# Kernel tuning notes

Hardware: AMD Instinct MI355X
Metric: run time of the kernel (lower is better)

## Reference

```python
import jax, jax.numpy as jnp
import numpy as np

# Static config (matches init_kwargs)
B, T, D = 4, 2048, 1024
E = 8            # num_experts
K = 2            # top_k
S = 1            # num_shared_experts
H = 1408         # expert_hidden_dim = round_to(4*1024//(K+S), 64)
N = B * T        # 8192 tokens
CAPACITY = 2560  # ceil(1.25 * K * N / E)
AUX_COEF = 0.01


def setup_inputs() -> dict:
    key = jax.random.key(0)
    ks = jax.random.split(key, 6)
    s = 1024 ** -0.5
    return {
        "x": jax.random.normal(ks[0], (B, T, D), jnp.float32),
        "router_weight": jax.random.normal(ks[1], (E, D), jnp.float32) * 0.02,
        "w_fc": jax.random.normal(ks[2], (E, D, H), jnp.float32) * s,
        "w_proj": jax.random.normal(ks[3], (E, H, D), jnp.float32) * s,
        "ws_fc": jax.random.normal(ks[4], (S, D, H), jnp.float32) * s,
        "ws_proj": jax.random.normal(ks[5], (S, H, D), jnp.float32) * s,
    }


def reference(x, router_weight, w_fc, w_proj, ws_fc, ws_proj):
    x_flat = x.reshape(N, D)

    # Shared experts: relu(x @ ws_fc)^2 @ ws_proj, summed over S experts
    h_s = jnp.square(jax.nn.relu(jnp.einsum("nd,sdh->snh", x_flat, ws_fc)))
    shared_out = jnp.einsum("snh,shd->nd", h_s, ws_proj)

    # Router: softmax in fp32, top-k, renormalize
    router_logits = x_flat @ router_weight.T                 # [N, E]
    routing_probs = jax.nn.softmax(router_logits.astype(jnp.float32), axis=-1)
    topk_probs, topk_idx = jax.lax.top_k(routing_probs, K)   # [N, K]
    topk_probs = topk_probs / (jnp.sum(topk_probs, axis=-1, keepdims=True) + 1e-9)
    topk_probs = topk_probs.astype(x.dtype)

    # Aux load-balancing loss (f uses top-1 assignment, no grad)
    f = jax.lax.stop_gradient(
        jnp.mean(jax.nn.one_hot(topk_idx[:, 0], E, dtype=routing_probs.dtype), axis=0))
    p = jnp.mean(routing_probs, axis=0)
    aux_loss = AUX_COEF * float(E) * jnp.sum(f * p)

    # Capacity-based dispatch: stable sort assignments by expert id
    flat_idx = topk_idx.reshape(-1)                          # [N*K]
    flat_probs = topk_probs.reshape(-1)                      # [N*K]
    flat_tok = jnp.repeat(jnp.arange(N, dtype=jnp.int32), K)  # [N*K]
    order = jnp.argsort(flat_idx, stable=True)
    sorted_idx = flat_idx[order]
    sorted_tok = flat_tok[order]
    sorted_probs = flat_probs[order]

    counts = jnp.zeros((E,), jnp.int32).at[flat_idx].add(1)
    starts = jnp.concatenate([jnp.zeros((1,), jnp.int32), jnp.cumsum(counts[:-1])])
    pos_within = jnp.arange(N * K, dtype=jnp.int32) - starts[sorted_idx]
    keep = (pos_within < CAPACITY).astype(x.dtype)
    pos_clamped = jnp.minimum(pos_within, CAPACITY - 1)
    slot = sorted_idx * CAPACITY + pos_clamped               # [N*K] -> E*CAPACITY buffer

    # Scatter tokens into per-expert capacity buffers (dropped tokens zeroed by keep)
    expert_inputs = jnp.zeros((E * CAPACITY, D), x.dtype).at[slot].add(
        x_flat[sorted_tok] * keep[:, None])
    expert_inputs = expert_inputs.reshape(E, CAPACITY, D)

    # Grouped expert FFN: relu(.)^2 MLP per expert
    hidden = jnp.square(jax.nn.relu(jnp.einsum("ecd,edh->ech", expert_inputs, w_fc)))
    expert_output = jnp.einsum("ech,ehd->ecd", hidden, w_proj).reshape(E * CAPACITY, D)

    # Gather + weighted scatter-combine back to tokens
    gathered = expert_output[slot]                           # [N*K, D]
    weighted = gathered * (sorted_probs * keep)[:, None]
    routed_out = jnp.zeros((N, D), x.dtype).at[sorted_tok].add(weighted)

    y = (routed_out + shared_out).reshape(B, T, D)
    return y, aux_loss
```

## Files before the change

### kernel.cpp

```cpp
#include <hip/hip_runtime.h>


#define NTOK 8192
#define DDIM 1024
#define HDIM 1408
#define CAP  2560
#define NROWS (NTOK + 8*CAP)
#define YN   8388608

typedef __bf16 bf16x8 __attribute__((ext_vector_type(8)));
typedef float  f32x4  __attribute__((ext_vector_type(4)));

typedef __attribute__((address_space(1))) void gvoid_t;
typedef __attribute__((address_space(3))) void svoid_t;

static __device__ __forceinline__ void load_lds16(const void* g, void* l) {
  __builtin_amdgcn_global_load_lds((gvoid_t*)g, (svoid_t*)l, 16, 0, 0);
}

__global__ __launch_bounds__(256) void zero_kernel(float* __restrict__ y,
                                                   float* __restrict__ psum,
                                                   int* __restrict__ fcnt) {
  size_t idx = (size_t)blockIdx.x * 256 + threadIdx.x;
  float4 z = make_float4(0.f, 0.f, 0.f, 0.f);
  float4* p = (float4*)y;
#pragma unroll
  for (int j = 0; j < 4; ++j) p[idx + (size_t)j * 524288] = z;
  if (idx == 0) {
    y[YN] = 0.f;
    for (int e = 0; e < 8; ++e) { psum[e] = 0.f; fcnt[e] = 0; }
  }
}

__global__ __launch_bounds__(256) void tconv_kernel(const float* __restrict__ in,
                                                    __bf16* __restrict__ out, int R, int C) {
  __shared__ float t[32][33];
  size_t mo = (size_t)blockIdx.z * R * C;
  const float* ip = in + mo;
  __bf16* op = out + mo;
  int c0 = blockIdx.x * 32, r0 = blockIdx.y * 32;
  int tx = threadIdx.x, ty = threadIdx.y;
#pragma unroll
  for (int k2 = 0; k2 < 4; ++k2)
    t[ty + k2 * 8][tx] = ip[(size_t)(r0 + ty + k2 * 8) * C + c0 + tx];
  __syncthreads();
#pragma unroll
  for (int k2 = 0; k2 < 4; ++k2)
    op[(size_t)(c0 + ty + k2 * 8) * R + r0 + tx] = (__bf16)t[tx][ty + k2 * 8];
}

__global__ __launch_bounds__(256) void router_kernel(
    const float* __restrict__ x, const float* __restrict__ rw,
    __bf16* __restrict__ xbf,
    int2* __restrict__ e01, float2* __restrict__ p01,
    int* __restrict__ tok_row, float* __restrict__ scale_row,
    float* __restrict__ psum, int* __restrict__ fcnt) {
  __shared__ float rwl[8 * 1024];
  __shared__ float ps[8];
  __shared__ int fc[8];
  int tid = threadIdx.x;
  if (tid < 8) { ps[tid] = 0.f; fc[tid] = 0; }
  float4* rl4 = (float4*)rwl;
  const float4* rg4 = (const float4*)rw;
#pragma unroll
  for (int j = 0; j < 8; ++j) rl4[tid + 256 * j] = rg4[tid + 256 * j];
  __syncthreads();
  int lane = tid & 63, wid = tid >> 6;
  for (int it = 0; it < 8; ++it) {
    int t = blockIdx.x * 32 + wid * 8 + it;
    const float4* xt = (const float4*)(x + (size_t)t * DDIM);
    float a[8];
#pragma unroll
    for (int e = 0; e < 8; ++e) a[e] = 0.f;
    float4 v[4];
#pragma unroll
    for (int jj = 0; jj < 4; ++jj) {
      v[jj] = xt[lane * 4 + jj];
#pragma unroll
      for (int e = 0; e < 8; ++e) {
        float4 w = rl4[e * 256 + lane * 4 + jj];
        a[e] += v[jj].x * w.x + v[jj].y * w.y + v[jj].z * w.z + v[jj].w * w.w;
      }
    }
    {
      bf16x8 o0, o1;
#pragma unroll
      for (int jj = 0; jj < 2; ++jj) {
        o0[jj * 4 + 0] = (__bf16)v[jj].x; o0[jj * 4 + 1] = (__bf16)v[jj].y;
        o0[jj * 4 + 2] = (__bf16)v[jj].z; o0[jj * 4 + 3] = (__bf16)v[jj].w;
        o1[jj * 4 + 0] = (__bf16)v[jj + 2].x; o1[jj * 4 + 1] = (__bf16)v[jj + 2].y;
        o1[jj * 4 + 2] = (__bf16)v[jj + 2].z; o1[jj * 4 + 3] = (__bf16)v[jj + 2].w;
      }
      __bf16* xo = xbf + (size_t)t * DDIM + lane * 16;
      *(bf16x8*)xo = o0;
      *(bf16x8*)(xo + 8) = o1;
    }
#pragma unroll
    for (int off = 32; off >= 1; off >>= 1)
#pragma unroll
      for (int e = 0; e < 8; ++e) a[e] += __shfl_xor(a[e], off);
    if (lane == 0) {
      int am = 0; float m = a[0];
      for (int e = 1; e < 8; ++e) if (a[e] > m) { m = a[e]; am = e; }
      float s = 0.f, ex[8];
      for (int e = 0; e < 8; ++e) { ex[e] = expf(a[e] - m); s += ex[e]; }
      float inv = 1.f / s;
      int am2 = -1; float m2 = -3.4e38f;
      for (int e = 0; e < 8; ++e) if (e != am && a[e] > m2) { m2 = a[e]; am2 = e; }
      float p0 = ex[am] * inv, p1 = ex[am2] * inv;
      float rn = 1.f / (p0 + p1 + 1e-9f);
      e01[t] = make_int2(am, am2);
      p01[t] = make_float2(p0 * rn, p1 * rn);
      tok_row[t] = t;
      scale_row[t] = 1.f;
      atomicAdd(&fc[am], 1);
      for (int e = 0; e < 8; ++e) atomicAdd(&ps[e], ex[e] * inv);
    }
  }
  __syncthreads();
  if (tid < 8) { atomicAdd(&psum[tid], ps[tid]); atomicAdd(&fcnt[tid], fc[tid]); }
}

__global__ __launch_bounds__(256) void dispatch_kernel(
    const int2* __restrict__ e01, const float2* __restrict__ p01,
    int* __restrict__ tok_row, float* __restrict__ scale_row, int* __restrict__ counts) {
  __shared__ int lcnt[256][8];
  int tid = threadIdx.x;
  int my[8];
#pragma unroll
  for (int e = 0; e < 8; ++e) my[e] = 0;
  int base = tid * 64;
  for (int j = 0; j < 64; ++j) {
    int ent = base + j; int t = ent >> 1;
    int2 ee = e01[t];
    int ex = (ent & 1) ? ee.y : ee.x;
    my[ex]++;
  }
#pragma unroll
  for (int e = 0; e < 8; ++e) lcnt[tid][e] = my[e];
  __syncthreads();
  if (tid < 8) {
    int run = 0;
    for (int i = 0; i < 256; ++i) { int c = lcnt[i][tid]; lcnt[i][tid] = run; run += c; }
    counts[tid] = run < CAP ? run : CAP;
  }
  __syncthreads();
  int offs[8];
#pragma unroll
  for (int e = 0; e < 8; ++e) offs[e] = lcnt[tid][e];
  for (int j = 0; j < 64; ++j) {
    int ent = base + j; int t = ent >> 1; int k = ent & 1;
    int2 ee = e01[t];
    int ex = k ? ee.y : ee.x;
    float pr = k ? p01[t].y : p01[t].x;
    int pos = offs[ex]++;
    if (pos < CAP) {
      int row = NTOK + ex * CAP + pos;
      tok_row[row] = t;
      scale_row[row] = pr;
    }
  }
}

template <int KD, int NDT, bool GATHER, int EPI>
__global__ __launch_bounds__(256, 4) void gemm_kernel(
    const __bf16* __restrict__ A, const __bf16* __restrict__ B,
    __bf16* __restrict__ Hout, float* __restrict__ Yout,
    const int* __restrict__ counts, const int* __restrict__ tok_row,
    const float* __restrict__ scale_row) {
  constexpr int NCT = NDT / 128;
  constexpr int SH = NTOK / 128;
  constexpr int ET = CAP / 128;
  int nwg = gridDim.x;
  int lin = (blockIdx.x & 7) * (nwg >> 3) + (blockIdx.x >> 3);
  int rem = lin % (4 * NCT);
  int rt = (lin / (4 * NCT)) * 4 + (rem & 3);
  int ct = rem >> 2;

  int g, i0, rowbase;
  if (rt < SH) { g = 8; rowbase = 0; i0 = rt << 7; }
  else { int r = rt - SH; g = r / ET; i0 = (r % ET) << 7; rowbase = NTOK + g * CAP; }
  int cnt = (g == 8) ? NTOK : counts[g];
  if (i0 >= cnt) return;

  __shared__ __align__(16) __bf16 As[128 * 64];
  __shared__ __align__(16) __bf16 Bs[128 * 64];
  __shared__ int   toksL[128];
  __shared__ float sclL[128];

  int tid = threadIdx.x, lane = tid & 63, wid = tid >> 6;

  if (tid < 128) {
    int i = i0 + tid; if (i > cnt - 1) i = cnt - 1;
    toksL[tid] = tok_row[rowbase + i];
    if (EPI == 2) sclL[tid] = scale_row[rowbase + i];
  }
  __syncthreads();

  int rsub = lane >> 3, csub = lane & 7;
  int csw = (csub ^ rsub) * 16;
  const char* aP[4];
  const char* bP[4];
  const char* Bg = (const char*)B + (size_t)g * NDT * KD * 2;
#pragma unroll
  for (int t = 0; t < 4; ++t) {
    int ia = wid * 32 + t * 8 + rsub;
    size_t arow = GATHER ? (size_t)toksL[ia] : (size_t)(rowbase + i0 + ia);
    aP[t] = (const char*)A + arow * (size_t)(KD * 2) + csw;
    int ib = ct * 128 + wid * 32 + t * 8 + rsub;
    bP[t] = Bg + (size_t)ib * (KD * 2) + csw;
  }

  f32x4 acc[4][4];
#pragma unroll
  for (int m2 = 0; m2 < 4; ++m2)
#pragma unroll
    for (int n2 = 0; n2 < 4; ++n2) acc[m2][n2] = f32x4{0.f, 0.f, 0.f, 0.f};

  int wr = wid >> 1, wc = wid & 1;
  int rA[4], rB[4], cS[2];
#pragma unroll
  for (int m2 = 0; m2 < 4; ++m2) rA[m2] = (wr * 64 + m2 * 16 + (lane & 15)) * 64;
#pragma unroll
  for (int n2 = 0; n2 < 4; ++n2) rB[n2] = (wc * 64 + n2 * 16 + (lane & 15)) * 64;
#pragma unroll
  for (int kk = 0; kk < 2; ++kk) cS[kk] = ((kk * 4 + (lane >> 4)) ^ (lane & 7)) * 8;

  for (int k0 = 0; k0 < KD; k0 += 64) {
    size_t kb = (size_t)k0 * 2;
#pragma unroll
    for (int t = 0; t < 4; ++t) {
      load_lds16(aP[t] + kb, &As[(wid * 32 + t * 8) * 64]);
      load_lds16(bP[t] + kb, &Bs[(wid * 32 + t * 8) * 64]);
    }
    __syncthreads();
#pragma unroll
    for (int kk = 0; kk < 2; ++kk) {
      bf16x8 af[4], bfr[4];
#pragma unroll
      for (int m2 = 0; m2 < 4; ++m2) af[m2] = *(const bf16x8*)&As[rA[m2] + cS[kk]];
#pragma unroll
      for (int n2 = 0; n2 < 4; ++n2) bfr[n2] = *(const bf16x8*)&Bs[rB[n2] + cS[kk]];
#pragma unroll
      for (int m2 = 0; m2 < 4; ++m2)
#pragma unroll
        for (int n2 = 0; n2 < 4; ++n2)
          acc[m2][n2] = __builtin_amdgcn_mfma_f32_16x16x32_bf16(af[m2], bfr[n2], acc[m2][n2], 0, 0, 0);
    }
    __syncthreads();
  }

#pragma unroll
  for (int m2 = 0; m2 < 4; ++m2) {
    int rb = wr * 64 + m2 * 16 + ((lane >> 4) << 2);
#pragma unroll
    for (int n2 = 0; n2 < 4; ++n2) {
      int col = ct * 128 + wc * 64 + n2 * 16 + (lane & 15);
#pragma unroll
      for (int r = 0; r < 4; ++r) {
        int grow = i0 + rb + r;
        if (grow < cnt) {
          float v = acc[m2][n2][r];
          if constexpr (EPI == 1) {
            v = fmaxf(v, 0.f);
            Hout[(size_t)(rowbase + grow) * NDT + col] = (__bf16)(v * v);
          } else {
            atomicAdd(&Yout[(size_t)toksL[rb + r] * NDT + col], v * sclL[rb + r]);
          }
        }
      }
    }
  }
}

__global__ void aux_kernel(const float* __restrict__ psum, const int* __restrict__ fcnt,
                           float* __restrict__ out) {
  float s = 0.f;
  for (int e = 0; e < 8; ++e) s += ((float)fcnt[e] / 8192.f) * (psum[e] / 8192.f);
  *out = 0.08f * s;
}

extern "C" void kernel_launch(void* const* d_in, const int* in_sizes, int n_in,
                              void* d_out, int out_size, void* d_ws, size_t ws_size,
                              hipStream_t stream) {
  const float* x      = (const float*)d_in[0];
  const float* rw     = (const float*)d_in[1];
  const float* wfc    = (const float*)d_in[2];
  const float* wproj  = (const float*)d_in[3];
  const float* wsfc   = (const float*)d_in[4];
  const float* wsproj = (const float*)d_in[5];
  float* y = (float*)d_out;

  char* ws = (char*)d_ws;
  size_t off = 0;
  auto alloc = [&](size_t bytes) {
    void* p = ws + off;
    off += (bytes + 1023) & ~(size_t)1023;
    return p;
  };
  __bf16* xbf      = (__bf16*)alloc((size_t)NTOK * DDIM * 2);
  __bf16* B1       = (__bf16*)alloc((size_t)9 * HDIM * DDIM * 2);
  __bf16* B2       = (__bf16*)alloc((size_t)9 * DDIM * HDIM * 2);
  __bf16* H        = (__bf16*)alloc((size_t)NROWS * HDIM * 2);
  int*    tok_row  = (int*)alloc((size_t)NROWS * 4);
  float*  scale_row= (float*)alloc((size_t)NROWS * 4);
  int2*   e01      = (int2*)alloc((size_t)NTOK * 8);
  float2* p01      = (float2*)alloc((size_t)NTOK * 8);
  int*    counts   = (int*)alloc(1024);
  float*  psum     = (float*)alloc(1024);
  int*    fcnt     = (int*)alloc(1024);
  (void)ws_size; (void)out_size; (void)in_sizes; (void)n_in;

  zero_kernel<<<2048, 256, 0, stream>>>(y, psum, fcnt);
  dim3 tb(32, 8);
  tconv_kernel<<<dim3(44, 32, 8), tb, 0, stream>>>(wfc, B1, 1024, 1408);
  tconv_kernel<<<dim3(44, 32, 1), tb, 0, stream>>>(wsfc, B1 + (size_t)8 * HDIM * DDIM, 1024, 1408);
  tconv_kernel<<<dim3(32, 44, 8), tb, 0, stream>>>(wproj, B2, 1408, 1024);
  tconv_kernel<<<dim3(32, 44, 1), tb, 0, stream>>>(wsproj, B2 + (size_t)8 * DDIM * HDIM, 1408, 1024);
  router_kernel<<<256, 256, 0, stream>>>(x, rw, xbf, e01, p01, tok_row, scale_row, psum, fcnt);
  dispatch_kernel<<<1, 256, 0, stream>>>(e01, p01, tok_row, scale_row, counts);
  gemm_kernel<1024, 1408, true, 1><<<2464, 256, 0, stream>>>(
      xbf, B1, H, nullptr, counts, tok_row, scale_row);
  gemm_kernel<1408, 1024, false, 2><<<1792, 256, 0, stream>>>(
      H, B2, nullptr, y, counts, tok_row, scale_row);
  aux_kernel<<<1, 1, 0, stream>>>(psum, fcnt, y + YN);
}
```

Baseline: 319.4 us.

## Fuse zero, weight conversion, router and aux into fewer launches

Merges output zeroing, the four weight transpose/convert launches and the router into a single block-indexed prep kernel. Global atomics on psum/fcnt become per-block partial writes, which the dispatch kernel reduces before also computing the aux loss, so the separate aux kernel goes away. This cuts kernel-launch gaps and lets the independent prep work share the GPU at once. The cost is a 32KB static LDS allocation for every block, which can limit occupancy for the small transpose blocks, and a serial 256-entry reduction inside the single-block dispatch kernel.

```diff
diff --git a/kernel.cpp b/kernel.cpp
--- a/kernel.cpp
+++ b/kernel.cpp
@@ -18,114 +18,148 @@
   __builtin_amdgcn_global_load_lds((gvoid_t*)g, (svoid_t*)l, 16, 0, 0);
 }
 
-__global__ __launch_bounds__(256) void zero_kernel(float* __restrict__ y,
-                                                   float* __restrict__ psum,
-                                                   int* __restrict__ fcnt) {
-  size_t idx = (size_t)blockIdx.x * 256 + threadIdx.x;
-  float4 z = make_float4(0.f, 0.f, 0.f, 0.f);
-  float4* p = (float4*)y;
-#pragma unroll
-  for (int j = 0; j < 4; ++j) p[idx + (size_t)j * 524288] = z;
-  if (idx == 0) {
-    y[YN] = 0.f;
-    for (int e = 0; e < 8; ++e) { psum[e] = 0.f; fcnt[e] = 0; }
-  }
-}
-
-__global__ __launch_bounds__(256) void tconv_kernel(const float* __restrict__ in,
-                                                    __bf16* __restrict__ out, int R, int C) {
-  __shared__ float t[32][33];
-  size_t mo = (size_t)blockIdx.z * R * C;
-  const float* ip = in + mo;
-  __bf16* op = out + mo;
-  int c0 = blockIdx.x * 32, r0 = blockIdx.y * 32;
-  int tx = threadIdx.x, ty = threadIdx.y;
+__device__ __forceinline__ void tconv_body(const float* __restrict__ in,
+                                           __bf16* __restrict__ out,
+                                           int R, int C, int bx, int by,
+                                           float* shbuf, int tid) {
+  float (*t)[33] = (float(*)[33])shbuf;
+  int c0 = bx * 32, r0 = by * 32;
+  int tx = tid & 31, ty = tid >> 5;
 #pragma unroll
   for (int k2 = 0; k2 < 4; ++k2)
-    t[ty + k2 * 8][tx] = ip[(size_t)(r0 + ty + k2 * 8) * C + c0 + tx];
+    t[ty + k2 * 8][tx] = in[(size_t)(r0 + ty + k2 * 8) * C + c0 + tx];
   __syncthreads();
 #pragma unroll
   for (int k2 = 0; k2 < 4; ++k2)
-    op[(size_t)(c0 + ty + k2 * 8) * R + r0 + tx] = (__bf16)t[tx][ty + k2 * 8];
-}
-
-__global__ __launch_bounds__(256) void router_kernel(
+    out[(size_t)(c0 + ty + k2 * 8) * R + r0 + tx] = (__bf16)t[tx][ty + k2 * 8];
+}
+
+__global__ __launch_bounds__(256) void prep_kernel(
     const float* __restrict__ x, const float* __restrict__ rw,
     __bf16* __restrict__ xbf,
     int2* __restrict__ e01, float2* __restrict__ p01,
     int* __restrict__ tok_row, float* __restrict__ scale_row,
-    float* __restrict__ psum, int* __restrict__ fcnt) {
-  __shared__ float rwl[8 * 1024];
+    float* __restrict__ psum_part, int* __restrict__ fcnt_part,
+    const float* __restrict__ wfc, const float* __restrict__ wsfc,
+    const float* __restrict__ wproj, const float* __restrict__ wsproj,
+    __bf16* __restrict__ B1, __bf16* __restrict__ B2,
+    float* __restrict__ y) {
+  __shared__ float shbuf[8192];
   __shared__ float ps[8];
   __shared__ int fc[8];
-  int tid = threadIdx.x;
-  if (tid < 8) { ps[tid] = 0.f; fc[tid] = 0; }
-  float4* rl4 = (float4*)rwl;
-  const float4* rg4 = (const float4*)rw;
-#pragma unroll
-  for (int j = 0; j < 8; ++j) rl4[tid + 256 * j] = rg4[tid + 256 * j];
-  __syncthreads();
-  int lane = tid & 63, wid = tid >> 6;
-  for (int it = 0; it < 8; ++it) {
-    int t = blockIdx.x * 32 + wid * 8 + it;
-    const float4* xt = (const float4*)(x + (size_t)t * DDIM);
-    float a[8];
-#pragma unroll
-    for (int e = 0; e < 8; ++e) a[e] = 0.f;
-    float4 v[4];
-#pragma unroll
-    for (int jj = 0; jj < 4; ++jj) {
-      v[jj] = xt[lane * 4 + jj];
-#pragma unroll
-      for (int e = 0; e < 8; ++e) {
-        float4 w = rl4[e * 256 + lane * 4 + jj];
-        a[e] += v[jj].x * w.x + v[jj].y * w.y + v[jj].z * w.z + v[jj].w * w.w;
+  int b = blockIdx.x, tid = threadIdx.x;
+
+  if (b < 256) {
+    if (tid < 8) { ps[tid] = 0.f; fc[tid] = 0; }
+    float4* rl4 = (float4*)shbuf;
+    const float4* rg4 = (const float4*)rw;
+#pragma unroll
+    for (int j = 0; j < 8; ++j) rl4[tid + 256 * j] = rg4[tid + 256 * j];
+    __syncthreads();
+    int lane = tid & 63, wid = tid >> 6;
+    for (int it = 0; it < 8; ++it) {
+      int t = b * 32 + wid * 8 + it;
+      const float4* xt = (const float4*)(x + (size_t)t * DDIM);
+      float a[8];
+#pragma unroll
+      for (int e = 0; e < 8; ++e) a[e] = 0.f;
+      float4 v[4];
+#pragma unroll
+      for (int jj = 0; jj < 4; ++jj) {
+        v[jj] = xt[lane * 4 + jj];
+#pragma unroll
+        for (int e = 0; e < 8; ++e) {
+          float4 w = rl4[e * 256 + lane * 4 + jj];
+          a[e] += v[jj].x * w.x + v[jj].y * w.y + v[jj].z * w.z + v[jj].w * w.w;
+        }
       }
-    }
-    {
-      bf16x8 o0, o1;
-#pragma unroll
-      for (int jj = 0; jj < 2; ++jj) {
-        o0[jj * 4 + 0] = (__bf16)v[jj].x; o0[jj * 4 + 1] = (__bf16)v[jj].y;
-        o0[jj * 4 + 2] = (__bf16)v[jj].z; o0[jj * 4 + 3] = (__bf16)v[jj].w;
-        o1[jj * 4 + 0] = (__bf16)v[jj + 2].x; o1[jj * 4 + 1] = (__bf16)v[jj + 2].y;
-        o1[jj * 4 + 2] = (__bf16)v[jj + 2].z; o1[jj * 4 + 3] = (__bf16)v[jj + 2].w;
+      {
+        bf16x8 o0, o1;
+#pragma unroll
+        for (int jj = 0; jj < 2; ++jj) {
+          o0[jj * 4 + 0] = (__bf16)v[jj].x; o0[jj * 4 + 1] = (__bf16)v[jj].y;
+          o0[jj * 4 + 2] = (__bf16)v[jj].z; o0[jj * 4 + 3] = (__bf16)v[jj].w;
+          o1[jj * 4 + 0] = (__bf16)v[jj + 2].x; o1[jj * 4 + 1] = (__bf16)v[jj + 2].y;
+          o1[jj * 4 + 2] = (__bf16)v[jj + 2].z; o1[jj * 4 + 3] = (__bf16)v[jj + 2].w;
+        }
+        __bf16* xo = xbf + (size_t)t * DDIM + lane * 16;
+        *(bf16x8*)xo = o0;
+        *(bf16x8*)(xo + 8) = o1;
       }
-      __bf16* xo = xbf + (size_t)t * DDIM + lane * 16;
-      *(bf16x8*)xo = o0;
-      *(bf16x8*)(xo + 8) = o1;
-    }
-#pragma unroll
-    for (int off = 32; off >= 1; off >>= 1)
-#pragma unroll
-      for (int e = 0; e < 8; ++e) a[e] += __shfl_xor(a[e], off);
-    if (lane == 0) {
-      int am = 0; float m = a[0];
-      for (int e = 1; e < 8; ++e) if (a[e] > m) { m = a[e]; am = e; }
-      float s = 0.f, ex[8];
-      for (int e = 0; e < 8; ++e) { ex[e] = expf(a[e] - m); s += ex[e]; }
-      float inv = 1.f / s;
-      int am2 = -1; float m2 = -3.4e38f;
-      for (int e = 0; e < 8; ++e) if (e != am && a[e] > m2) { m2 = a[e]; am2 = e; }
-      float p0 = ex[am] * inv, p1 = ex[am2] * inv;
-      float rn = 1.f / (p0 + p1 + 1e-9f);
-      e01[t] = make_int2(am, am2);
-      p01[t] = make_float2(p0 * rn, p1 * rn);
-      tok_row[t] = t;
-      scale_row[t] = 1.f;
-      atomicAdd(&fc[am], 1);
-      for (int e = 0; e < 8; ++e) atomicAdd(&ps[e], ex[e] * inv);
-    }
-  }
-  __syncthreads();
-  if (tid < 8) { atomicAdd(&psum[tid], ps[tid]); atomicAdd(&fcnt[tid], fc[tid]); }
+#pragma unroll
+      for (int off = 32; off >= 1; off >>= 1)
+#pragma unroll
+        for (int e = 0; e < 8; ++e) a[e] += __shfl_xor(a[e], off);
+      if (lane == 0) {
+        int am = 0; float m = a[0];
+        for (int e = 1; e < 8; ++e) if (a[e] > m) { m = a[e]; am = e; }
+        float s = 0.f, ex[8];
+        for (int e = 0; e < 8; ++e) { ex[e] = expf(a[e] - m); s += ex[e]; }
+        float inv = 1.f / s;
+        int am2 = -1; float m2 = -3.4e38f;
+        for (int e = 0; e < 8; ++e) if (e != am && a[e] > m2) { m2 = a[e]; am2 = e; }
+        float p0 = ex[am] * inv, p1 = ex[am2] * inv;
+        float rn = 1.f / (p0 + p1 + 1e-9f);
+        e01[t] = make_int2(am, am2);
+        p01[t] = make_float2(p0 * rn, p1 * rn);
+        tok_row[t] = t;
+        scale_row[t] = 1.f;
+        atomicAdd(&fc[am], 1);
+        for (int e = 0; e < 8; ++e) atomicAdd(&ps[e], ex[e] * inv);
+      }
+    }
+    __syncthreads();
+    if (tid < 8) { psum_part[b * 8 + tid] = ps[tid]; fcnt_part[b * 8 + tid] = fc[tid]; }
+    return;
+  }
+  b -= 256;
+  if (b < 2048) {
+    size_t idx = (size_t)b * 256 + tid;
+    float4 z = make_float4(0.f, 0.f, 0.f, 0.f);
+    float4* p = (float4*)y;
+#pragma unroll
+    for (int j = 0; j < 4; ++j) p[idx + (size_t)j * 524288] = z;
+    return;
+  }
+  b -= 2048;
+  if (b < 11264) {
+    int e = b / 1408, r = b % 1408;
+    tconv_body(wfc + (size_t)e * 1024 * 1408, B1 + (size_t)e * HDIM * DDIM,
+               1024, 1408, r % 44, r / 44, shbuf, tid);
+    return;
+  }
+  b -= 11264;
+  if (b < 1408) {
+    tconv_body(wsfc, B1 + (size_t)8 * HDIM * DDIM, 1024, 1408, b % 44, b / 44, shbuf, tid);
+    return;
+  }
+  b -= 1408;
+  if (b < 11264) {
+    int e = b / 1408, r = b % 1408;
+    tconv_body(wproj + (size_t)e * 1408 * 1024, B2 + (size_t)e * DDIM * HDIM,
+               1408, 1024, r % 32, r / 32, shbuf, tid);
+    return;
+  }
+  b -= 11264;
+  {
+    tconv_body(wsproj, B2 + (size_t)8 * DDIM * HDIM, 1408, 1024, b % 32, b / 32, shbuf, tid);
+  }
 }
 
 __global__ __launch_bounds__(256) void dispatch_kernel(
     const int2* __restrict__ e01, const float2* __restrict__ p01,
-    int* __restrict__ tok_row, float* __restrict__ scale_row, int* __restrict__ counts) {
+    int* __restrict__ tok_row, float* __restrict__ scale_row, int* __restrict__ counts,
+    const float* __restrict__ psum_part, const int* __restrict__ fcnt_part,
+    float* __restrict__ aux_out) {
   __shared__ int lcnt[256][8];
+  __shared__ float aps[8];
+  __shared__ int afc[8];
   int tid = threadIdx.x;
+  if (tid < 8) {
+    float s = 0.f; int c = 0;
+    for (int i = 0; i < 256; ++i) { s += psum_part[i * 8 + tid]; c += fcnt_part[i * 8 + tid]; }
+    aps[tid] = s; afc[tid] = c;
+  }
   int my[8];
 #pragma unroll
   for (int e = 0; e < 8; ++e) my[e] = 0;
@@ -159,6 +193,11 @@
       tok_row[row] = t;
       scale_row[row] = pr;
     }
+  }
+  if (tid == 0) {
+    float s = 0.f;
+    for (int e = 0; e < 8; ++e) s += ((float)afc[e] / 8192.f) * (aps[e] / 8192.f);
+    *aux_out = 0.08f * s;
   }
 }
 
@@ -271,13 +310,6 @@
       }
     }
   }
-}
-
-__global__ void aux_kernel(const float* __restrict__ psum, const int* __restrict__ fcnt,
-                           float* __restrict__ out) {
-  float s = 0.f;
-  for (int e = 0; e < 8; ++e) s += ((float)fcnt[e] / 8192.f) * (psum[e] / 8192.f);
-  *out = 0.08f * s;
 }
 
 extern "C" void kernel_launch(void* const* d_in, const int* in_sizes, int n_in,
@@ -307,21 +339,17 @@
   int2*   e01      = (int2*)alloc((size_t)NTOK * 8);
   float2* p01      = (float2*)alloc((size_t)NTOK * 8);
   int*    counts   = (int*)alloc(1024);
-  float*  psum     = (float*)alloc(1024);
-  int*    fcnt     = (int*)alloc(1024);
+  float*  psum_part= (float*)alloc(256 * 8 * 4);
+  int*    fcnt_part= (int*)alloc(256 * 8 * 4);
   (void)ws_size; (void)out_size; (void)in_sizes; (void)n_in;
 
-  zero_kernel<<<2048, 256, 0, stream>>>(y, psum, fcnt);
-  dim3 tb(32, 8);
-  tconv_kernel<<<dim3(44, 32, 8), tb, 0, stream>>>(wfc, B1, 1024, 1408);
-  tconv_kernel<<<dim3(44, 32, 1), tb, 0, stream>>>(wsfc, B1 + (size_t)8 * HDIM * DDIM, 1024, 1408);
-  tconv_kernel<<<dim3(32, 44, 8), tb, 0, stream>>>(wproj, B2, 1408, 1024);
-  tconv_kernel<<<dim3(32, 44, 1), tb, 0, stream>>>(wsproj, B2 + (size_t)8 * DDIM * HDIM, 1408, 1024);
-  router_kernel<<<256, 256, 0, stream>>>(x, rw, xbf, e01, p01, tok_row, scale_row, psum, fcnt);
-  dispatch_kernel<<<1, 256, 0, stream>>>(e01, p01, tok_row, scale_row, counts);
+  prep_kernel<<<27648, 256, 0, stream>>>(x, rw, xbf, e01, p01, tok_row, scale_row,
+                                         psum_part, fcnt_part,
+                                         wfc, wsfc, wproj, wsproj, B1, B2, y);
+  dispatch_kernel<<<1, 256, 0, stream>>>(e01, p01, tok_row, scale_row, counts,
+                                         psum_part, fcnt_part, y + YN);
   gemm_kernel<1024, 1408, true, 1><<<2464, 256, 0, stream>>>(
       xbf, B1, H, nullptr, counts, tok_row, scale_row);
   gemm_kernel<1408, 1024, false, 2><<<1792, 256, 0, stream>>>(
       H, B2, nullptr, y, counts, tok_row, scale_row);
-  aux_kernel<<<1, 1, 0, stream>>>(psum, fcnt, y + YN);
-}
+}
```

Measured after the change: 333.9 us. 4.5% more time.
